# Kernel optimization log

Hardware: AMD Instinct MI355X
Metric: run time of the kernel (lower is better)

Reference implementation:

```python
import jax, jax.numpy as jnp
import numpy as np

B, L, E, H = 2, 2048, 2048, 16
HD = E // H  # 128


def build_rope(length, head_dim, base=10000.0):
    # [L, head_dim//2, 2] with [..., 0]=sin, [..., 1]=cos (matches apply_rope indexing)
    half = head_dim // 2
    inv_freq = 1.0 / (base ** (jnp.arange(half, dtype=jnp.float32) * 2.0 / head_dim))
    ang = jnp.arange(length, dtype=jnp.float32)[:, None] * inv_freq[None, :]  # [L, half]
    return jnp.stack([jnp.sin(ang), jnp.cos(ang)], axis=-1)  # [L, half, 2]


def apply_rope(x, rope):
    # x: [B, L, H, D]; rope: [L, D//2, 2] (sin, cos)
    b, l, h, d = x.shape
    sin = rope[:, :, 0].reshape(1, l, 1, d // 2)
    cos = rope[:, :, 1].reshape(1, l, 1, d // 2)
    xr = x.reshape(b, l, h, d // 2, 2)
    q0, q1 = xr[..., 0], xr[..., 1]
    out = jnp.stack([q0 * cos - q1 * sin, q1 * cos + q0 * sin], axis=-1)
    return out.reshape(b, l, h, d)


def setup_inputs() -> dict:
    key = jax.random.key(0)
    k1, k2, k3 = jax.random.split(key, 3)
    x = jax.random.normal(k1, (B, L, E), dtype=jnp.float32)
    w_attn = jax.random.normal(k2, (3 * E, E), dtype=jnp.float32) * (E ** -0.5)
    w_proj = jax.random.normal(k3, (E, E), dtype=jnp.float32) * (E ** -0.5)
    rope = build_rope(L, HD)
    return {"x": x, "rope": rope, "w_attn": w_attn, "w_proj": w_proj}


def reference(x, rope, w_attn, w_proj):
    b, l, e = x.shape
    h, hd = H, HD
    qkv = jnp.einsum('ble,fe->blf', x, w_attn)  # [B, L, 3E]
    q, k, v = jnp.split(qkv, 3, axis=-1)
    q = apply_rope(q.reshape(b, l, h, hd), rope)
    k = apply_rope(k.reshape(b, l, h, hd), rope)
    v = v.reshape(b, l, h, hd)
    # causal SDPA, scale 1/sqrt(head_dim)
    scale = 1.0 / np.sqrt(hd).astype(np.float32)
    scores = jnp.einsum('bqhd,bkhd->bhqk', q, k) * scale
    causal = jnp.tril(jnp.ones((l, l), dtype=bool))
    scores = jnp.where(causal[None, None], scores, jnp.finfo(scores.dtype).min)
    att = jax.nn.softmax(scores, axis=-1)
    y = jnp.einsum('bhqk,bkhd->bqhd', att, v).reshape(b, l, e)
    return jnp.einsum('ble,fe->blf', y, w_proj)
```

## Files before the change

### kernel.cpp

```cpp
#include <hip/hip_runtime.h>
#include <math.h>

#define BATCH 2
#define LSEQ  2048
#define EMB   2048
#define NH    16
#define HD    128

typedef __attribute__((ext_vector_type(8))) short bf16x8;
typedef __attribute__((ext_vector_type(8))) unsigned short u16x8;
typedef __attribute__((ext_vector_type(4))) float f32x4;

static __device__ __forceinline__ unsigned short f2bf(float f) {
    unsigned u = __float_as_uint(f);
    u += 0x7fffu + ((u >> 16) & 1u);
    return (unsigned short)(u >> 16);
}

static __device__ __forceinline__ void load_lds16(const void* g, void* l) {
    __builtin_amdgcn_global_load_lds(
        (const __attribute__((address_space(1))) void*)g,
        (__attribute__((address_space(3))) void*)l, 16, 0, 0);
}

#define N1 (BATCH * LSEQ * EMB)
#define N2 (3 * EMB * EMB)
#define N3 (EMB * EMB)

__global__ __launch_bounds__(256) void cast_bf16_kernel(
    const float* __restrict__ x, const float* __restrict__ wa,
    const float* __restrict__ wp,
    unsigned short* __restrict__ xb, unsigned short* __restrict__ wab,
    unsigned short* __restrict__ wpb)
{
    size_t i4 = ((size_t)blockIdx.x * 256 + threadIdx.x) * 4;
    const float* src;
    unsigned short* dst;
    size_t off;
    if (i4 < (size_t)N1) { src = x; dst = xb; off = i4; }
    else if (i4 < (size_t)N1 + N2) { src = wa; dst = wab; off = i4 - N1; }
    else { src = wp; dst = wpb; off = i4 - N1 - N2; }
    float4 f = *(const float4*)(src + off);
    ushort4 u;
    u.x = f2bf(f.x); u.y = f2bf(f.y); u.z = f2bf(f.z); u.w = f2bf(f.w);
    *(ushort4*)(dst + off) = u;
}

__global__ __launch_bounds__(256) void gemm_bt_bf16(
    const unsigned short* __restrict__ A, const unsigned short* __restrict__ B,
    const float* __restrict__ rope,
    float* __restrict__ C,
    unsigned short* __restrict__ qo, unsigned short* __restrict__ ko,
    unsigned short* __restrict__ vo,
    int M, int N, int K, int mode)
{
    __shared__ unsigned short As[128 * 64];
    __shared__ unsigned short Bs[128 * 64];

    const int tid = threadIdx.x;
    const int lane = tid & 63;
    const int w = tid >> 6;
    const int m = lane & 15;
    const int g = lane >> 4;
    const int wm = (w & 1) * 64;
    const int wn = (w >> 1) * 64;
    const int bm = blockIdx.y * 128;
    const int bn = blockIdx.x * 128;

    f32x4 acc[4][4];
#pragma unroll
    for (int mi = 0; mi < 4; mi++)
#pragma unroll
        for (int ni = 0; ni < 4; ni++) acc[mi][ni] = (f32x4){0.f, 0.f, 0.f, 0.f};

    for (int k0 = 0; k0 < K; k0 += 64) {
        __syncthreads();
#pragma unroll
        for (int i = 0; i < 4; i++) {
            const int idx = i * 256 + tid;
            const int row = idx >> 3;
            const int c = (idx & 7) ^ (row & 7);
            load_lds16(A + (size_t)(bm + row) * K + k0 + c * 8, &As[idx * 8]);
            load_lds16(B + (size_t)(bn + row) * K + k0 + c * 8, &Bs[idx * 8]);
        }
        __syncthreads();

#pragma unroll
        for (int kc = 0; kc < 2; kc++) {
            bf16x8 af[4], bfv[4];
#pragma unroll
            for (int mi = 0; mi < 4; mi++) {
                const int row = wm + mi * 16 + m;
                af[mi] = *(const bf16x8*)&As[(row * 8 + ((kc * 4 + g) ^ (m & 7))) * 8];
            }
#pragma unroll
            for (int ni = 0; ni < 4; ni++) {
                const int row = wn + ni * 16 + m;
                bfv[ni] = *(const bf16x8*)&Bs[(row * 8 + ((kc * 4 + g) ^ (m & 7))) * 8];
            }
#pragma unroll
            for (int mi = 0; mi < 4; mi++)
#pragma unroll
                for (int ni = 0; ni < 4; ni++)
                    acc[mi][ni] = __builtin_amdgcn_mfma_f32_16x16x32_bf16(
                        af[mi], bfv[ni], acc[mi][ni], 0, 0, 0);
        }
    }

#pragma unroll
    for (int mi = 0; mi < 4; mi++) {
#pragma unroll
        for (int ni = 0; ni < 4; ni++) {
            const int col = bn + wn + ni * 16 + m;
            if (mode == 0) {
#pragma unroll
                for (int r = 0; r < 4; r++) {
                    const int row = bm + wm + mi * 16 + g * 4 + r;
                    C[(size_t)row * N + col] = acc[mi][ni][r];
                }
            } else {
                const int which = col >> 11;
                const int e = col & 2047;
                const int h = e >> 7;
                const int d = e & 127;
                if (which < 2) {
                    unsigned short* dst = (which == 0) ? qo : ko;
                    const int t2 = ((d >> 1) << 1);
#pragma unroll
                    for (int r = 0; r < 4; r++) {
                        const int row = bm + wm + mi * 16 + g * 4 + r;
                        const int b = row >> 11;
                        const int l = row & 2047;
                        float val = acc[mi][ni][r];
                        const float prt = __shfl_xor(val, 1);
                        const float2 sc = *(const float2*)(rope + (size_t)l * HD + t2);
                        val = (m & 1) ? fmaf(val, sc.y, prt * sc.x)
                                      : fmaf(val, sc.y, -prt * sc.x);
                        dst[(((size_t)(b * NH + h)) * LSEQ + l) * HD + d] = f2bf(val);
                    }
                } else {
                    const int l0 = bm + wm + mi * 16 + g * 4;
                    const int b = l0 >> 11;
                    const int l = l0 & 2047;
                    ushort4 vv;
                    vv.x = f2bf(acc[mi][ni][0]);
                    vv.y = f2bf(acc[mi][ni][1]);
                    vv.z = f2bf(acc[mi][ni][2]);
                    vv.w = f2bf(acc[mi][ni][3]);
                    *(ushort4*)(vo + (((size_t)(b * NH + h)) * HD + d) * LSEQ + l) = vv;
                }
            }
        }
    }
}

#define PTILES 32
#define PS_STR 68

__global__ __launch_bounds__(256) void attn_kernel(
    const unsigned short* __restrict__ q, const unsigned short* __restrict__ k,
    const unsigned short* __restrict__ vT, unsigned short* __restrict__ y)
{
    __shared__ unsigned short Ks[64 * 128];
    __shared__ unsigned short Vs[128 * 64];
    __shared__ unsigned short Ps[64 * PS_STR];

    const int tid = threadIdx.x;
    const int lane = tid & 63;
    const int w = tid >> 6;
    const int m = lane & 15;
    const int g = lane >> 4;
    const int bx = blockIdx.x;
    const int qt = (bx & 1) ? (PTILES - 1 - (bx >> 1)) : (bx >> 1);
    const int bh = blockIdx.y;
    const int q0 = qt * 64;
    const size_t base = (size_t)bh * LSEQ * HD;
    const float scale = 0.08838834764831845f;
    const int bB = bh / NH;
    const int hh = bh % NH;
    const int sw = m & 7;

    bf16x8 aq[4];
    {
        const unsigned short* qrow = q + base + (size_t)(q0 + w * 16 + m) * HD;
#pragma unroll
        for (int kc = 0; kc < 4; kc++)
            aq[kc] = *(const bf16x8*)(qrow + kc * 32 + g * 8);
    }

    f32x4 o[8];
#pragma unroll
    for (int i = 0; i < 8; i++) o[i] = (f32x4){0.f, 0.f, 0.f, 0.f};
    float mprev[4], lsum[4];
#pragma unroll
    for (int r = 0; r < 4; r++) { mprev[r] = -1e30f; lsum[r] = 0.f; }

    for (int kt = 0; kt <= qt; kt++) {
        const int k0 = kt * 64;

        __syncthreads();
        {
            const unsigned short* ksrc = k + base + (size_t)k0 * HD;
#pragma unroll
            for (int i = 0; i < 4; i++) {
                const int idx = i * 256 + tid;
                const int row = idx >> 4;
                const int c = (idx & 15) ^ (row & 7);
                load_lds16(ksrc + (size_t)row * HD + c * 8, &Ks[idx * 8]);
            }
        }
        {
#pragma unroll
            for (int i = 0; i < 4; i++) {
                const int idx = i * 256 + tid;
                const int d = idx >> 3;
                const int c = (idx & 7) ^ (d & 7);
                load_lds16(vT + base + (size_t)d * LSEQ + k0 + c * 8, &Vs[idx * 8]);
            }
        }
        __syncthreads();

        f32x4 s[4];
#pragma unroll
        for (int n = 0; n < 4; n++) {
            f32x4 acc = (f32x4){0.f, 0.f, 0.f, 0.f};
#pragma unroll
            for (int kc = 0; kc < 4; kc++) {
                const int row = n * 16 + m;
                bf16x8 bk = *(const bf16x8*)&Ks[(row * 16 + ((kc * 4 + g) ^ sw)) * 8];
                acc = __builtin_amdgcn_mfma_f32_16x16x32_bf16(aq[kc], bk, acc, 0, 0, 0);
            }
            s[n] = acc;
        }

        const int rowg = q0 + w * 16 + g * 4;
        if (kt == qt) {
#pragma unroll
            for (int n = 0; n < 4; n++) {
                const int col = k0 + n * 16 + m;
#pragma unroll
                for (int r = 0; r < 4; r++) {
                    const float val = s[n][r] * scale;
                    s[n][r] = (col <= rowg + r) ? val : -1e30f;
                }
            }
        } else {
#pragma unroll
            for (int n = 0; n < 4; n++)
#pragma unroll
                for (int r = 0; r < 4; r++) s[n][r] *= scale;
        }

        float al[4];
#pragma unroll
        for (int r = 0; r < 4; r++) {
            float v0 = fmaxf(fmaxf(s[0][r], s[1][r]), fmaxf(s[2][r], s[3][r]));
            v0 = fmaxf(v0, __shfl_xor(v0, 1));
            v0 = fmaxf(v0, __shfl_xor(v0, 2));
            v0 = fmaxf(v0, __shfl_xor(v0, 4));
            v0 = fmaxf(v0, __shfl_xor(v0, 8));
            const float mn = fmaxf(mprev[r], v0);
            al[r] = __expf(mprev[r] - mn);
            mprev[r] = mn;
        }
#pragma unroll
        for (int r = 0; r < 4; r++) {
            float sum = 0.f;
#pragma unroll
            for (int n = 0; n < 4; n++) {
                const float p = __expf(s[n][r] - mprev[r]);
                sum += p;
                Ps[(w * 16 + g * 4 + r) * PS_STR + n * 16 + m] = f2bf(p);
            }
            sum += __shfl_xor(sum, 1);
            sum += __shfl_xor(sum, 2);
            sum += __shfl_xor(sum, 4);
            sum += __shfl_xor(sum, 8);
            lsum[r] = lsum[r] * al[r] + sum;
        }

#pragma unroll
        for (int dc = 0; dc < 8; dc++)
#pragma unroll
            for (int r = 0; r < 4; r++) o[dc][r] *= al[r];

        bf16x8 ap[2];
#pragma unroll
        for (int kk = 0; kk < 2; kk++)
            ap[kk] = *(const bf16x8*)&Ps[(w * 16 + m) * PS_STR + kk * 32 + g * 8];
#pragma unroll
        for (int dc = 0; dc < 8; dc++) {
#pragma unroll
            for (int kk = 0; kk < 2; kk++) {
                const int row = dc * 16 + m;
                bf16x8 bv = *(const bf16x8*)&Vs[(row * 8 + ((kk * 4 + g) ^ sw)) * 8];
                o[dc] = __builtin_amdgcn_mfma_f32_16x16x32_bf16(ap[kk], bv, o[dc], 0, 0, 0);
            }
        }
    }

#pragma unroll
    for (int r = 0; r < 4; r++) {
        const float inv = 1.f / lsum[r];
        const int lrow = q0 + w * 16 + g * 4 + r;
        unsigned short* dst = y + (((size_t)bB * LSEQ + lrow) * NH + hh) * HD;
#pragma unroll
        for (int dc = 0; dc < 8; dc++)
            dst[dc * 16 + m] = f2bf(o[dc][r] * inv);
    }
}

extern "C" void kernel_launch(void* const* d_in, const int* in_sizes, int n_in,
                              void* d_out, int out_size, void* d_ws, size_t ws_size,
                              hipStream_t stream) {
    const float* x      = (const float*)d_in[0];
    const float* rope   = (const float*)d_in[1];
    const float* w_attn = (const float*)d_in[2];
    const float* w_proj = (const float*)d_in[3];
    float* out = (float*)d_out;
    unsigned short* ws = (unsigned short*)d_ws;

    const size_t per = (size_t)BATCH * NH * LSEQ * HD;
    unsigned short* qb  = ws;
    unsigned short* kb  = ws + per;
    unsigned short* vb  = ws + 2 * per;
    unsigned short* yb  = ws + 3 * per;
    unsigned short* xb  = ws + 4 * per;
    unsigned short* wab = xb + (size_t)N1;
    unsigned short* wpb = wab + (size_t)N2;

    const int M = BATCH * LSEQ;

    const int cast_blocks = (N1 + N2 + N3) / 4 / 256;
    cast_bf16_kernel<<<cast_blocks, 256, 0, stream>>>(x, w_attn, w_proj, xb, wab, wpb);

    dim3 g1(3 * EMB / 128, M / 128);
    gemm_bt_bf16<<<g1, 256, 0, stream>>>(xb, wab, rope, nullptr, qb, kb, vb,
                                         M, 3 * EMB, EMB, 1);

    dim3 ga(PTILES, BATCH * NH);
    attn_kernel<<<ga, 256, 0, stream>>>(qb, kb, vb, yb);

    dim3 g2(EMB / 128, M / 128);
    gemm_bt_bf16<<<g2, 256, 0, stream>>>(yb, wpb, nullptr, out,
                                         nullptr, nullptr, nullptr, M, EMB, EMB, 0);
}
```

Baseline: 468.4 us.

## Double-buffer K/V tiles in attention and swizzle GEMM block order across XCDs

```diff
diff --git a/kernel.cpp b/kernel.cpp
--- a/kernel.cpp
+++ b/kernel.cpp
@@ -64,8 +64,13 @@
     const int g = lane >> 4;
     const int wm = (w & 1) * 64;
     const int wn = (w >> 1) * 64;
-    const int bm = blockIdx.y * 128;
-    const int bn = blockIdx.x * 128;
+
+    const int nwgx = gridDim.x;
+    const int lin = blockIdx.y * nwgx + blockIdx.x;
+    const int cpx = (nwgx * gridDim.y) >> 3;
+    const int swz = (lin & 7) * cpx + (lin >> 3);
+    const int bm = (swz / nwgx) * 128;
+    const int bn = (swz % nwgx) * 128;
 
     f32x4 acc[4][4];
 #pragma unroll
@@ -161,18 +166,17 @@
     const unsigned short* __restrict__ q, const unsigned short* __restrict__ k,
     const unsigned short* __restrict__ vT, unsigned short* __restrict__ y)
 {
-    __shared__ unsigned short Ks[64 * 128];
-    __shared__ unsigned short Vs[128 * 64];
-    __shared__ unsigned short Ps[64 * PS_STR];
+    __shared__ __align__(16) unsigned short Ks[2][64 * 128];
+    __shared__ __align__(16) unsigned short Vs[2][64 * 128];
+    __shared__ __align__(16) unsigned short Ps[64 * PS_STR];
 
     const int tid = threadIdx.x;
     const int lane = tid & 63;
     const int w = tid >> 6;
     const int m = lane & 15;
     const int g = lane >> 4;
-    const int bx = blockIdx.x;
-    const int qt = (bx & 1) ? (PTILES - 1 - (bx >> 1)) : (bx >> 1);
-    const int bh = blockIdx.y;
+    const int bh = blockIdx.x;
+    const int qt = PTILES - 1 - blockIdx.y;
     const int q0 = qt * 64;
     const size_t base = (size_t)bh * LSEQ * HD;
     const float scale = 0.08838834764831845f;
@@ -180,6 +184,24 @@
     const int hh = bh % NH;
     const int sw = m & 7;
 
+    auto stage = [&](int buf, int kb0) {
+        const unsigned short* ksrc = k + base + (size_t)kb0 * HD;
+#pragma unroll
+        for (int i = 0; i < 4; i++) {
+            const int idx = i * 256 + tid;
+            const int row = idx >> 4;
+            const int c = (idx & 15) ^ (row & 7);
+            load_lds16(ksrc + (size_t)row * HD + c * 8, &Ks[buf][idx * 8]);
+        }
+#pragma unroll
+        for (int i = 0; i < 4; i++) {
+            const int idx = i * 256 + tid;
+            const int d = idx >> 3;
+            const int c = (idx & 7) ^ (d & 7);
+            load_lds16(vT + base + (size_t)d * LSEQ + kb0 + c * 8, &Vs[buf][idx * 8]);
+        }
+    };
+
     bf16x8 aq[4];
     {
         const unsigned short* qrow = q + base + (size_t)(q0 + w * 16 + m) * HD;
@@ -195,30 +217,18 @@
 #pragma unroll
     for (int r = 0; r < 4; r++) { mprev[r] = -1e30f; lsum[r] = 0.f; }
 
+    stage(0, 0);
+    int cur = 0;
+
     for (int kt = 0; kt <= qt; kt++) {
         const int k0 = kt * 64;
 
         __syncthreads();
-        {
-            const unsigned short* ksrc = k + base + (size_t)k0 * HD;
-#pragma unroll
-            for (int i = 0; i < 4; i++) {
-                const int idx = i * 256 + tid;
-                const int row = idx >> 4;
-                const int c = (idx & 15) ^ (row & 7);
-                load_lds16(ksrc + (size_t)row * HD + c * 8, &Ks[idx * 8]);
-            }
-        }
-        {
-#pragma unroll
-            for (int i = 0; i < 4; i++) {
-                const int idx = i * 256 + tid;
-                const int d = idx >> 3;
-                const int c = (idx & 7) ^ (d & 7);
-                load_lds16(vT + base + (size_t)d * LSEQ + k0 + c * 8, &Vs[idx * 8]);
-            }
-        }
-        __syncthreads();
+
+        if (kt < qt) stage(cur ^ 1, k0 + 64);
+
+        const unsigned short* Kc = Ks[cur];
+        const unsigned short* Vc = Vs[cur];
 
         f32x4 s[4];
 #pragma unroll
@@ -227,7 +237,7 @@
 #pragma unroll
             for (int kc = 0; kc < 4; kc++) {
                 const int row = n * 16 + m;
-                bf16x8 bk = *(const bf16x8*)&Ks[(row * 16 + ((kc * 4 + g) ^ sw)) * 8];
+                bf16x8 bk = *(const bf16x8*)&Kc[(row * 16 + ((kc * 4 + g) ^ sw)) * 8];
                 acc = __builtin_amdgcn_mfma_f32_16x16x32_bf16(aq[kc], bk, acc, 0, 0, 0);
             }
             s[n] = acc;
@@ -293,10 +303,12 @@
 #pragma unroll
             for (int kk = 0; kk < 2; kk++) {
                 const int row = dc * 16 + m;
-                bf16x8 bv = *(const bf16x8*)&Vs[(row * 8 + ((kk * 4 + g) ^ sw)) * 8];
+                bf16x8 bv = *(const bf16x8*)&Vc[(row * 8 + ((kk * 4 + g) ^ sw)) * 8];
                 o[dc] = __builtin_amdgcn_mfma_f32_16x16x32_bf16(ap[kk], bv, o[dc], 0, 0, 0);
             }
         }
+
+        cur ^= 1;
     }
 
 #pragma unroll
@@ -338,7 +350,7 @@
     gemm_bt_bf16<<<g1, 256, 0, stream>>>(xb, wab, rope, nullptr, qb, kb, vb,
                                          M, 3 * EMB, EMB, 1);
 
-    dim3 ga(PTILES, BATCH * NH);
+    dim3 ga(BATCH * NH, PTILES);
     attn_kernel<<<ga, 256, 0, stream>>>(qb, kb, vb, yb);
 
     dim3 g2(EMB / 128, M / 128);
```

Result: faster. 407.1 us (-13.1%).
